# Optimization experiments

Hardware: AMD Instinct MI355X
Metric: run time of the kernel (lower is better)

The kernel has to match this reference:

```python
import jax, jax.numpy as jnp
import numpy as np

B, L, E, H = 4, 4096, 1024, 16
DH = E // H          # 64 head dim
R, M, P = 1, 8, 16   # quadrature nodes, prf features, poly sketch dim
EPS = 1e-6
C = 2.0 + EPS


def setup_inputs() -> dict:
    key = jax.random.key(0)
    ks = jax.random.split(key, 10)
    x = jax.random.normal(ks[0], (B, L, E), dtype=jnp.float32)
    qkv_w = jax.random.normal(ks[1], (E, 3 * E), dtype=jnp.float32) * 0.02
    qkv_b = jnp.zeros((3 * E,), dtype=jnp.float32)
    out_w = jax.random.normal(ks[2], (E, E), dtype=jnp.float32) * 0.02
    out_b = jnp.zeros((E,), dtype=jnp.float32)
    omega = jax.random.normal(ks[3], (R, H, DH, M), dtype=jnp.float32)
    ts_hash1 = jax.random.randint(ks[4], (DH,), 0, P)
    ts_sign1 = jax.random.randint(ks[5], (DH,), 0, 2) * 2 - 1
    ts_hash2 = jax.random.randint(ks[6], (DH,), 0, P)
    ts_sign2 = jax.random.randint(ks[7], (DH,), 0, 2) * 2 - 1
    # laggauss(1): node=1.0, weight=1.0
    quad_nodes = jnp.array([1.0], dtype=jnp.float32) / C
    quad_weights = jnp.array([1.0], dtype=jnp.float32) / C
    return {"x": x, "qkv_w": qkv_w, "qkv_b": qkv_b, "out_w": out_w,
            "out_b": out_b, "omega": omega, "quad_nodes": quad_nodes,
            "quad_weights": quad_weights, "ts_hash1": ts_hash1,
            "ts_sign1": ts_sign1, "ts_hash2": ts_hash2, "ts_sign2": ts_sign2}


def _safe_normalize(x, eps=1e-6):
    norm = jnp.linalg.norm(x, axis=-1, keepdims=True)
    return x / jnp.clip(norm, eps)


def _count_sketch(x, h, s):
    # x: (B,H,L,DH); h,s: (DH,) int
    vals = x * s.astype(x.dtype)
    Mhot = jax.nn.one_hot(h, P, dtype=x.dtype)  # (DH, P)
    return jnp.dot(vals, Mhot)                  # (B,H,L,P)


def _poly_tensor_sketch(x, h1, s1, h2, s2):
    cs1 = _count_sketch(x, h1, s1)
    cs2 = _count_sketch(x, h2, s2)
    f1 = jnp.fft.rfft(cs1, axis=-1)
    f2 = jnp.fft.rfft(cs2, axis=-1)
    ts = jnp.fft.irfft(f1 * f2, n=P, axis=-1)
    return ts / jnp.sqrt(float(P))


def _prf_features(x, omega, quad_nodes):
    proj = jnp.einsum('bhld,rhdm->rbhlm', x, omega)
    s_vals = quad_nodes.reshape(-1, 1, 1, 1, 1)
    sqrt_2s = jnp.sqrt(2.0 * jnp.clip(s_vals, 0.0))
    exp_arg = jnp.clip(proj * sqrt_2s - s_vals, -10.0, 10.0)
    return jnp.exp(exp_arg) / jnp.sqrt(float(M))


def reference(x, qkv_w, qkv_b, out_w, out_b, omega, quad_nodes, quad_weights,
              ts_hash1, ts_sign1, ts_hash2, ts_sign2):
    qkv = x @ qkv_w + qkv_b
    q, k, v = jnp.split(qkv, 3, axis=-1)
    q = q.reshape(B, L, H, DH).transpose(0, 2, 1, 3)
    k = k.reshape(B, L, H, DH).transpose(0, 2, 1, 3)
    v = v.reshape(B, L, H, DH).transpose(0, 2, 1, 3)

    q_norm = _safe_normalize(q)
    k_norm = _safe_normalize(k)

    q_poly = _poly_tensor_sketch(q_norm, ts_hash1, ts_sign1, ts_hash2, ts_sign2)
    k_poly = _poly_tensor_sketch(k_norm, ts_hash1, ts_sign1, ts_hash2, ts_sign2)
    q_prf = _prf_features(q_norm, omega, quad_nodes)
    k_prf = _prf_features(k_norm, omega, quad_nodes)

    sq_w = jnp.sqrt(jnp.clip(quad_weights.reshape(-1, 1, 1, 1, 1), 0.0))
    q_prf = q_prf * sq_w
    k_prf = k_prf * sq_w

    q_fuse = jnp.einsum('bhlp,rbhlm->bhlrpm', q_poly, q_prf).reshape(B, H, L, -1)
    k_fuse = jnp.einsum('bhlp,rbhlm->bhlrpm', k_poly, k_prf).reshape(B, H, L, -1)

    kv = jnp.einsum('bhlf,bhld->bhfd', k_fuse, v)
    context = jnp.einsum('bhlf,bhfd->bhld', q_fuse, kv)
    k_sum = k_fuse.sum(axis=2)                              # (B,H,F)
    norm = jnp.einsum('bhlf,bhf->bhl', q_fuse, k_sum)
    output = context / jnp.clip(norm, 0.0001)[..., None]

    output = output.transpose(0, 2, 1, 3).reshape(B, L, E)
    return output @ out_w + out_b
```

## Files before the change

kernel.cpp:

```cpp
#include <hip/hip_runtime.h>

typedef unsigned short u16;
typedef __attribute__((ext_vector_type(8))) short bfrag8;
typedef __attribute__((ext_vector_type(4))) float f32x4;

__device__ __forceinline__ float b2f(u16 u){ union { unsigned ui; float f; } v; v.ui = ((unsigned)u) << 16; return v.f; }
__device__ __forceinline__ u16 f2b(float f){ union { float f; unsigned ui; } v; v.f = f; unsigned r = (v.ui + 0x7FFF + ((v.ui >> 16) & 1)) >> 16; return (u16)r; }

__global__ __launch_bounds__(256) void zero_f32(float* p, int n){
  int i = blockIdx.x*256 + threadIdx.x;
  if (i < n) p[i] = 0.f;
}

__global__ __launch_bounds__(256) void transpose_f32(const float* __restrict__ W, float* __restrict__ Wt, int K, int N){
  __shared__ float tile[32][33];
  int bx = blockIdx.x * 32, by = blockIdx.y * 32;
  int tx = threadIdx.x & 31, ty = threadIdx.x >> 5;
  #pragma unroll
  for (int i = 0; i < 32; i += 8) tile[ty+i][tx] = W[(size_t)(by+ty+i)*N + bx+tx];
  __syncthreads();
  #pragma unroll
  for (int i = 0; i < 32; i += 8) Wt[(size_t)(bx+ty+i)*K + by+tx] = tile[tx][ty+i];
}

__global__ __launch_bounds__(256) void transpose_f2b(const float* __restrict__ W, u16* __restrict__ Wt, int K, int N){
  __shared__ u16 tile[32][33];
  int bx = blockIdx.x * 32, by = blockIdx.y * 32;
  int tx = threadIdx.x & 31, ty = threadIdx.x >> 5;
  #pragma unroll
  for (int i = 0; i < 32; i += 8) tile[ty+i][tx] = f2b(W[(size_t)(by+ty+i)*N + bx+tx]);
  __syncthreads();
  #pragma unroll
  for (int i = 0; i < 32; i += 8) Wt[(size_t)(bx+ty+i)*K + by+tx] = tile[tx][ty+i];
}

template<int NS>
__device__ __forceinline__ void stage_split(u16* lds, int off, const float* __restrict__ src){
  float v[8];
  *(float4*)v       = *(const float4*)src;
  *(float4*)(v + 4) = *(const float4*)(src + 4);
  u16 p0[8], p1[8];
  #pragma unroll
  for (int i = 0; i < 8; ++i){
    u16 a = f2b(v[i]); p0[i] = a;
    if constexpr (NS > 1){ p1[i] = f2b(v[i] - b2f(a)); }
  }
  *(uint4*)(lds + off) = *(uint4*)p0;
  if constexpr (NS > 1) *(uint4*)(lds + 4096 + off) = *(uint4*)p1;
}

template<int NPROD>
__global__ __launch_bounds__(256) void gemm_split(
    const float* __restrict__ A, int lda,
    const float* __restrict__ Bt, int bn_off,
    const float* __restrict__ bias,
    float* __restrict__ Cq, float* __restrict__ Ck, u16* __restrict__ Cv, int K)
{
  constexpr int NSA = (NPROD==3) ? 2 : 1;
  __shared__ __align__(16) u16 As[NSA*4096];
  __shared__ __align__(16) u16 Bs[NSA*4096];
  int tid = threadIdx.x, lane = tid & 63, wave = tid >> 6;
  int wm = wave >> 1, wn = wave & 1;
  int bm = blockIdx.y * 128, bn = blockIdx.x * 128;
  f32x4 acc[4][4];
  #pragma unroll
  for (int i=0;i<4;i++)
    #pragma unroll
    for (int j=0;j<4;j++)
      #pragma unroll
      for (int r=0;r<4;r++) acc[i][j][r] = 0.f;
  int mr = lane & 15, kq = (lane >> 4) * 8;
  for (int k0 = 0; k0 < K; k0 += 32) {
    #pragma unroll
    for (int v = 0; v < 2; ++v) {
      int idx = tid + v*256;
      int row = idx >> 2, col = (idx & 3) * 8;
      stage_split<NSA>(As, row*32 + col, &A [(size_t)(bm+row)*lda + k0 + col]);
      stage_split<NSA>(Bs, row*32 + col, &Bt[(size_t)(bn_off+bn+row)*K + k0 + col]);
    }
    __syncthreads();
    bfrag8 af[NSA][4], bf[NSA][4];
    #pragma unroll
    for (int s=0;s<NSA;s++){
      #pragma unroll
      for (int i=0;i<4;i++) af[s][i] = *(const bfrag8*)(&As[s*4096 + (wm*64 + i*16 + mr)*32 + kq]);
      #pragma unroll
      for (int j=0;j<4;j++) bf[s][j] = *(const bfrag8*)(&Bs[s*4096 + (wn*64 + j*16 + mr)*32 + kq]);
    }
#define MM(sa,sb) \
    { _Pragma("unroll") for (int i=0;i<4;i++){ _Pragma("unroll") for (int j=0;j<4;j++){ \
        acc[i][j] = __builtin_amdgcn_mfma_f32_16x16x32_bf16(af[sa][i], bf[sb][j], acc[i][j], 0, 0, 0); } } }
    if constexpr (NPROD == 3){ MM(0,1) MM(1,0) }
    MM(0,0)
#undef MM
    __syncthreads();
  }
  #pragma unroll
  for (int i=0;i<4;i++){
    #pragma unroll
    for (int j=0;j<4;j++){
      int col = bn_off + bn + wn*64 + j*16 + (lane & 15);
      float bv = bias[col];
      #pragma unroll
      for (int r=0;r<4;r++){
        int row = bm + wm*64 + i*16 + (lane>>4)*4 + r;
        float val = acc[i][j][r] + bv;
        if (col < 1024)      Cq[(size_t)row*1024 + col]        = val;
        else if (col < 2048) Ck[(size_t)row*1024 + (col-1024)] = val;
        else                 Cv[(size_t)row*1024 + (col-2048)] = f2b(val);
      }
    }
  }
}

__global__ __launch_bounds__(256) void gemm_b16(const u16* __restrict__ A, int lda,
    const u16* __restrict__ Bt, const float* __restrict__ bias, float* __restrict__ C, int N, int K)
{
  __shared__ __align__(16) u16 As[4096];
  __shared__ __align__(16) u16 Bs[4096];
  int tid = threadIdx.x, lane = tid & 63, wave = tid >> 6;
  int wm = wave >> 1, wn = wave & 1;
  int bm = blockIdx.y * 128, bn = blockIdx.x * 128;
  f32x4 acc[4][4];
  #pragma unroll
  for (int i=0;i<4;i++)
    #pragma unroll
    for (int j=0;j<4;j++)
      #pragma unroll
      for (int r=0;r<4;r++) acc[i][j][r] = 0.f;
  int mr = lane & 15, kq = (lane >> 4) * 8;
  for (int k0 = 0; k0 < K; k0 += 32) {
    #pragma unroll
    for (int v = 0; v < 2; ++v) {
      int idx = tid + v*256;
      int row = idx >> 2, col = (idx & 3) * 8;
      *(uint4*)(&As[row*32 + col]) = *(const uint4*)(&A[(size_t)(bm+row)*lda + k0 + col]);
      *(uint4*)(&Bs[row*32 + col]) = *(const uint4*)(&Bt[(size_t)(bn+row)*K + k0 + col]);
    }
    __syncthreads();
    bfrag8 af[4], bf[4];
    #pragma unroll
    for (int i=0;i<4;i++) af[i] = *(const bfrag8*)(&As[(wm*64 + i*16 + mr)*32 + kq]);
    #pragma unroll
    for (int j=0;j<4;j++) bf[j] = *(const bfrag8*)(&Bs[(wn*64 + j*16 + mr)*32 + kq]);
    #pragma unroll
    for (int i=0;i<4;i++)
      #pragma unroll
      for (int j=0;j<4;j++)
        acc[i][j] = __builtin_amdgcn_mfma_f32_16x16x32_bf16(af[i], bf[j], acc[i][j], 0, 0, 0);
    __syncthreads();
  }
  #pragma unroll
  for (int i=0;i<4;i++){
    #pragma unroll
    for (int j=0;j<4;j++){
      int col = bn + wn*64 + j*16 + (lane & 15);
      float bv = bias[col];
      #pragma unroll
      for (int r=0;r<4;r++){
        int row = bm + wm*64 + i*16 + (lane>>4)*4 + r;
        C[(size_t)row*N + col] = acc[i][j][r] + bv;
      }
    }
  }
}

struct __align__(16) ConsT { int b1; float sg1; int b2; float sg2; };

#define FEATS_COMPUTE(TILE, TOKA)                                                \
  float sq = 0.f;                                                                \
  _Pragma("unroll")                                                              \
  for (int dd = 0; dd < 16; ++dd){ float u = TILE[(TOKA)*65 + g*16 + dd]; sq += u*u; } \
  sq += __shfl_xor(sq, 16); sq += __shfl_xor(sq, 32);                            \
  float sc = 1.f / fmaxf(sqrtf(sq), 1e-6f);                                      \
  float cs1[16], cs2[16], pm[8];                                                 \
  _Pragma("unroll") for (int p=0;p<16;p++){ cs1[p]=0.f; cs2[p]=0.f; }            \
  _Pragma("unroll") for (int m=0;m<8;m++) pm[m]=0.f;                             \
  _Pragma("unroll")                                                              \
  for (int dd = 0; dd < 16; ++dd){                                               \
    int d = g*16 + dd;                                                           \
    float un = TILE[(TOKA)*65 + d] * sc;                                         \
    ConsT cc = cons[d];                                                          \
    float v1 = un*cc.sg1, v2 = un*cc.sg2;                                        \
    _Pragma("unroll")                                                            \
    for (int p=0;p<16;p++){ cs1[p] += (cc.b1==p)?v1:0.f; cs2[p] += (cc.b2==p)?v2:0.f; } \
    _Pragma("unroll")                                                            \
    for (int m=0;m<8;m++) pm[m] += un * oms[d*8 + m];                            \
  }                                                                              \
  _Pragma("unroll")                                                              \
  for (int p=0;p<16;p++){ cs1[p] += __shfl_xor(cs1[p],16); cs1[p] += __shfl_xor(cs1[p],32); \
                          cs2[p] += __shfl_xor(cs2[p],16); cs2[p] += __shfl_xor(cs2[p],32); } \
  _Pragma("unroll")                                                              \
  for (int m=0;m<8;m++){ pm[m] += __shfl_xor(pm[m],16); pm[m] += __shfl_xor(pm[m],32); } \
  float poly4[4];                                                                \
  _Pragma("unroll")                                                              \
  for (int pi=0;pi<4;pi++){ int p = g*4 + pi; float s = 0.f;                     \
    _Pragma("unroll") for (int a=0;a<16;a++) s += cs1[a]*cs2[(p-a)&15];          \
    poly4[pi] = s * 0.25f; }                                                     \
  float prf[8];                                                                  \
  _Pragma("unroll")                                                              \
  for (int m=0;m<8;m++){ float e = fminf(fmaxf(pm[m]*sqrt2s - s_node, -10.f), 10.f); \
    prf[m] = expf(e) * pscale; }

__global__ __launch_bounds__(256) void kfeat_kv(const float* __restrict__ kf, const u16* __restrict__ vb,
    const float* __restrict__ omega, const float* __restrict__ qn, const float* __restrict__ qw,
    const int* __restrict__ h1, const int* __restrict__ s1,
    const int* __restrict__ h2, const int* __restrict__ s2,
    float* __restrict__ kvT, float* __restrict__ ksum)
{
  __shared__ float ktile[64*65];
  __shared__ __align__(16) u16 vtile[64*64];
  __shared__ __align__(16) u16 featT[128*72];
  __shared__ float oms[64*8];
  __shared__ ConsT cons[64];
  int tid = threadIdx.x, lane = tid & 63, wave = tid >> 6;
  int bh = blockIdx.y, b = bh >> 4, h = bh & 15;
  int chunk = blockIdx.x;
  if (tid < 64) {
    ConsT c; c.b1 = h1[tid]; c.sg1 = (float)s1[tid]; c.b2 = h2[tid]; c.sg2 = (float)s2[tid];
    cons[tid] = c;
  }
  for (int i = tid; i < 512; i += 256) oms[i] = omega[h*512 + i];
  float s_node = qn[0];
  float sqrt2s = sqrtf(2.f * fmaxf(s_node, 0.f));
  float pscale = 0.35355339059327373f * sqrtf(fmaxf(qw[0], 0.f));
  int tloc = lane & 15, g = lane >> 4;
  int tokA = wave*16 + tloc;
  int wm = wave >> 1, wn = wave & 1;
  int mr = lane & 15, kq8 = (lane >> 4) * 8;
  f32x4 acc[4][2];
  #pragma unroll
  for (int i=0;i<4;i++)
    #pragma unroll
    for (int jn=0;jn<2;jn++)
      #pragma unroll
      for (int r=0;r<4;r++) acc[i][jn][r] = 0.f;
  float kacc[32];
  #pragma unroll
  for (int j=0;j<32;j++) kacc[j] = 0.f;
  for (int sub = 0; sub < 8; ++sub) {
    int base = chunk*512 + sub*64;
    __syncthreads();
    for (int idx = tid; idx < 4096; idx += 256) {
      int t = idx >> 6, d = idx & 63;
      ktile[t*65 + d] = kf[(size_t)(b*4096 + base + t)*1024 + h*64 + d];
    }
    for (int slot = tid; slot < 512; slot += 256) {
      int t = slot >> 3, o = (slot & 7) * 8;
      *(uint4*)(&vtile[t*64 + o]) = *(const uint4*)(&vb[(size_t)(b*4096 + base + t)*1024 + h*64 + o]);
    }
    __syncthreads();
    {
      FEATS_COMPUTE(ktile, tokA)
      #pragma unroll
      for (int pi=0;pi<4;pi++){
        #pragma unroll
        for (int m=0;m<8;m++){
          int f = (g*4 + pi)*8 + m;
          float v = poly4[pi]*prf[m];
          featT[f*72 + tokA] = f2b(v);
          v += __shfl_xor(v,1); v += __shfl_xor(v,2); v += __shfl_xor(v,4); v += __shfl_xor(v,8);
          if (tloc == 0) kacc[pi*8 + m] += v;
        }
      }
    }
    __syncthreads();
    #pragma unroll
    for (int k0 = 0; k0 < 64; k0 += 32) {
      bfrag8 af[4];
      #pragma unroll
      for (int i=0;i<4;i++) af[i] = *(const bfrag8*)(&featT[(wm*64 + i*16 + mr)*72 + k0 + kq8]);
      #pragma unroll
      for (int jn=0;jn<2;jn++){
        int d = wn*32 + jn*16 + mr;
        short tmp[8];
        #pragma unroll
        for (int j=0;j<8;j++) tmp[j] = (short)vtile[(k0 + kq8 + j)*64 + d];
        bfrag8 bf = *(bfrag8*)tmp;
        #pragma unroll
        for (int i=0;i<4;i++)
          acc[i][jn] = __builtin_amdgcn_mfma_f32_16x16x32_bf16(af[i], bf, acc[i][jn], 0, 0, 0);
      }
    }
  }
  #pragma unroll
  for (int i=0;i<4;i++){
    #pragma unroll
    for (int jn=0;jn<2;jn++){
      int d = wn*32 + jn*16 + (lane & 15);
      #pragma unroll
      for (int r=0;r<4;r++){
        int f = wm*64 + i*16 + (lane>>4)*4 + r;
        atomicAdd(&kvT[((size_t)bh*64 + d)*128 + f], acc[i][jn][r]);
      }
    }
  }
  if (tloc == 0){
    #pragma unroll
    for (int j=0;j<32;j++) atomicAdd(&ksum[bh*128 + g*32 + j], kacc[j]);
  }
}

__global__ __launch_bounds__(256) void qfeat_ctx(const float* __restrict__ qf,
    const float* __restrict__ omega, const float* __restrict__ qn, const float* __restrict__ qw,
    const int* __restrict__ h1, const int* __restrict__ s1,
    const int* __restrict__ h2, const int* __restrict__ s2,
    const float* __restrict__ kvT, const float* __restrict__ ksum,
    u16* __restrict__ attn)
{
  __shared__ float qtile[64*65];
  __shared__ __align__(16) u16 feat[64*136];
  __shared__ __align__(16) u16 kvsb0[64*136];
  __shared__ __align__(16) u16 kvsb1[64*136];
  __shared__ float ksums[128];
  __shared__ float nrm_s[64];
  __shared__ float oms[64*8];
  __shared__ ConsT cons[64];
  int tid = threadIdx.x, lane = tid & 63, wave = tid >> 6;
  int bh = blockIdx.y, b = bh >> 4, h = bh & 15;
  int chunk = blockIdx.x;
  if (tid < 64) {
    ConsT c; c.b1 = h1[tid]; c.sg1 = (float)s1[tid]; c.b2 = h2[tid]; c.sg2 = (float)s2[tid];
    cons[tid] = c;
  }
  for (int i = tid; i < 512; i += 256) oms[i] = omega[h*512 + i];
  for (int idx = tid; idx < 8192; idx += 256) {
    int d = idx >> 7, f = idx & 127;
    float v = kvT[((size_t)bh*64 + d)*128 + f];
    u16 b0 = f2b(v);
    kvsb0[d*136 + f] = b0;
    kvsb1[d*136 + f] = f2b(v - b2f(b0));
  }
  if (tid < 128) ksums[tid] = ksum[bh*128 + tid];
  float s_node = qn[0];
  float sqrt2s = sqrtf(2.f * fmaxf(s_node, 0.f));
  float pscale = 0.35355339059327373f * sqrtf(fmaxf(qw[0], 0.f));
  int tloc = lane & 15, g = lane >> 4;
  int tokA = wave*16 + tloc;
  int mr = lane & 15, kq8 = (lane >> 4) * 8;
  for (int sub = 0; sub < 8; ++sub) {
    int base = chunk*512 + sub*64;
    for (int idx = tid; idx < 4096; idx += 256) {
      int t = idx >> 6, d = idx & 63;
      qtile[t*65 + d] = qf[(size_t)(b*4096 + base + t)*1024 + h*64 + d];
    }
    __syncthreads();
    {
      FEATS_COMPUTE(qtile, tokA)
      float nv = 0.f;
      #pragma unroll
      for (int pi=0;pi<4;pi++){
        #pragma unroll
        for (int m=0;m<8;m++){
          int f = (g*4 + pi)*8 + m;
          float v = poly4[pi]*prf[m];
          feat[tokA*136 + f] = f2b(v);
          nv += v * ksums[f];
        }
      }
      nv += __shfl_xor(nv, 16); nv += __shfl_xor(nv, 32);
      if (lane < 16) nrm_s[tokA] = nv;
    }
    __syncthreads();
    f32x4 cacc[4];
    #pragma unroll
    for (int jn=0;jn<4;jn++)
      #pragma unroll
      for (int r=0;r<4;r++) cacc[jn][r] = 0.f;
    #pragma unroll
    for (int k0 = 0; k0 < 128; k0 += 32) {
      bfrag8 af = *(const bfrag8*)(&feat[(wave*16 + mr)*136 + k0 + kq8]);
      #pragma unroll
      for (int jn=0;jn<4;jn++){
        int d = jn*16 + mr;
        bfrag8 b0 = *(const bfrag8*)(&kvsb0[d*136 + k0 + kq8]);
        cacc[jn] = __builtin_amdgcn_mfma_f32_16x16x32_bf16(af, b0, cacc[jn], 0, 0, 0);
        bfrag8 b1 = *(const bfrag8*)(&kvsb1[d*136 + k0 + kq8]);
        cacc[jn] = __builtin_amdgcn_mfma_f32_16x16x32_bf16(af, b1, cacc[jn], 0, 0, 0);
      }
    }
    #pragma unroll
    for (int jn=0;jn<4;jn++){
      int d = jn*16 + (lane & 15);
      #pragma unroll
      for (int r=0;r<4;r++){
        int row = (lane>>4)*4 + r;
        float nrm = nrm_s[wave*16 + row];
        int tok = base + wave*16 + row;
        attn[(size_t)(b*4096 + tok)*2048 + h*64 + d] = f2b(cacc[jn][r] / fmaxf(nrm, 1e-4f));
      }
    }
  }
}

extern "C" void kernel_launch(void* const* d_in, const int* in_sizes, int n_in,
                              void* d_out, int out_size, void* d_ws, size_t ws_size,
                              hipStream_t stream)
{
  const float* x     = (const float*)d_in[0];
  const float* qkv_w = (const float*)d_in[1];
  const float* qkv_b = (const float*)d_in[2];
  const float* out_w = (const float*)d_in[3];
  const float* out_b = (const float*)d_in[4];
  const float* omega = (const float*)d_in[5];
  const float* qn    = (const float*)d_in[6];
  const float* qw    = (const float*)d_in[7];
  const int* h1 = (const int*)d_in[8];
  const int* s1 = (const int*)d_in[9];
  const int* h2 = (const int*)d_in[10];
  const int* s2 = (const int*)d_in[11];

  const size_t SZ_Q   = (size_t)16384*1024*4;
  const size_t SZ_K   = (size_t)16384*1024*4;
  const size_t SZ_V   = (size_t)16384*1024*2;
  const size_t SZ_WT1 = (size_t)3072*1024*4;
  const size_t SZ_WT2 = (size_t)1024*1024*2;
  const size_t SZ_KV  = (size_t)64*64*128*4;
  char* ws = (char*)d_ws;
  float* qf  = (float*)ws;
  float* kf  = (float*)(ws + SZ_Q);
  u16*   vb  = (u16*)  (ws + SZ_Q + SZ_K);
  float* wT1 = (float*)(ws + SZ_Q + SZ_K + SZ_V);
  u16*   wT2 = (u16*)  (ws + SZ_Q + SZ_K + SZ_V + SZ_WT1);
  float* kvT = (float*)(ws + SZ_Q + SZ_K + SZ_V + SZ_WT1 + SZ_WT2);
  float* ksp = (float*)(ws + SZ_Q + SZ_K + SZ_V + SZ_WT1 + SZ_WT2 + SZ_KV);

  int nz = (int)((SZ_KV + (size_t)64*128*4) / 4);
  zero_f32<<<(nz+255)/256, 256, 0, stream>>>(kvT, nz);
  transpose_f32<<<dim3(3072/32, 1024/32), 256, 0, stream>>>(qkv_w, wT1, 1024, 3072);
  transpose_f2b<<<dim3(1024/32, 1024/32), 256, 0, stream>>>(out_w, wT2, 1024, 1024);
  gemm_split<3><<<dim3(16, 128), 256, 0, stream>>>(x, 1024, wT1, 0, qkv_b, qf, kf, vb, 1024);
  gemm_split<1><<<dim3(8, 128), 256, 0, stream>>>(x, 1024, wT1, 2048, qkv_b, qf, kf, vb, 1024);
  kfeat_kv<<<dim3(8, 64), 256, 0, stream>>>(kf, vb, omega, qn, qw, h1, s1, h2, s2, kvT, ksp);
  qfeat_ctx<<<dim3(8, 64), 256, 0, stream>>>(qf, omega, qn, qw, h1, s1, h2, s2, kvT, ksp, (u16*)kf);
  gemm_b16<<<dim3(8, 128), 256, 0, stream>>>((const u16*)kf, 2048, wT2, out_b, (float*)d_out, 1024, 1024);
}
```

Before: 1.062 ms.

## Pre-split x and weights into bf16 hi/lo planes, stage via global_load_lds

Adds prepass kernels that convert x and the transposed qkv weight into separate bf16 high and low planes once, rather than having every GEMM tile re-convert fp32 to split bf16 in registers. The GEMMs then stage tiles straight from global memory into LDS with global_load_lds 16-byte transfers, using a k-group-major LDS layout. The aim is less redundant conversion ALU work and fewer register round-trips during staging. The cost is extra prepass kernels and extra workspace traffic for the split planes.

```diff
diff --git a/kernel.cpp b/kernel.cpp
--- a/kernel.cpp
+++ b/kernel.cpp
@@ -7,12 +7,32 @@
 __device__ __forceinline__ float b2f(u16 u){ union { unsigned ui; float f; } v; v.ui = ((unsigned)u) << 16; return v.f; }
 __device__ __forceinline__ u16 f2b(float f){ union { float f; unsigned ui; } v; v.f = f; unsigned r = (v.ui + 0x7FFF + ((v.ui >> 16) & 1)) >> 16; return (u16)r; }
 
+__device__ __forceinline__ void gl_lds16(const u16* g, u16* l){
+  __builtin_amdgcn_global_load_lds(
+      (const __attribute__((address_space(1))) unsigned*)g,
+      (__attribute__((address_space(3))) unsigned*)l, 16, 0, 0);
+}
+
 __global__ __launch_bounds__(256) void zero_f32(float* p, int n){
   int i = blockIdx.x*256 + threadIdx.x;
   if (i < n) p[i] = 0.f;
 }
 
-__global__ __launch_bounds__(256) void transpose_f32(const float* __restrict__ W, float* __restrict__ Wt, int K, int N){
+__global__ __launch_bounds__(256) void split_x(const float* __restrict__ x,
+    u16* __restrict__ xh, u16* __restrict__ xl){
+  size_t i = ((size_t)blockIdx.x*256 + threadIdx.x) * 8;
+  float v[8];
+  *(float4*)v       = *(const float4*)(x + i);
+  *(float4*)(v + 4) = *(const float4*)(x + i + 4);
+  u16 h[8], l[8];
+  #pragma unroll
+  for (int j = 0; j < 8; ++j){ u16 a = f2b(v[j]); h[j] = a; l[j] = f2b(v[j] - b2f(a)); }
+  *(uint4*)(xh + i) = *(uint4*)h;
+  *(uint4*)(xl + i) = *(uint4*)l;
+}
+
+__global__ __launch_bounds__(256) void transpose_split(const float* __restrict__ W,
+    u16* __restrict__ Th, u16* __restrict__ Tl, int K, int N){
   __shared__ float tile[32][33];
   int bx = blockIdx.x * 32, by = blockIdx.y * 32;
   int tx = threadIdx.x & 31, ty = threadIdx.x >> 5;
@@ -20,7 +40,12 @@
   for (int i = 0; i < 32; i += 8) tile[ty+i][tx] = W[(size_t)(by+ty+i)*N + bx+tx];
   __syncthreads();
   #pragma unroll
-  for (int i = 0; i < 32; i += 8) Wt[(size_t)(bx+ty+i)*K + by+tx] = tile[tx][ty+i];
+  for (int i = 0; i < 32; i += 8){
+    float v = tile[tx][ty+i];
+    u16 h = f2b(v);
+    Th[(size_t)(bx+ty+i)*K + by+tx] = h;
+    Tl[(size_t)(bx+ty+i)*K + by+tx] = f2b(v - b2f(h));
+  }
 }
 
 __global__ __launch_bounds__(256) void transpose_f2b(const float* __restrict__ W, u16* __restrict__ Wt, int K, int N){
@@ -34,31 +59,16 @@
   for (int i = 0; i < 32; i += 8) Wt[(size_t)(bx+ty+i)*K + by+tx] = tile[tx][ty+i];
 }
 
-template<int NS>
-__device__ __forceinline__ void stage_split(u16* lds, int off, const float* __restrict__ src){
-  float v[8];
-  *(float4*)v       = *(const float4*)src;
-  *(float4*)(v + 4) = *(const float4*)(src + 4);
-  u16 p0[8], p1[8];
-  #pragma unroll
-  for (int i = 0; i < 8; ++i){
-    u16 a = f2b(v[i]); p0[i] = a;
-    if constexpr (NS > 1){ p1[i] = f2b(v[i] - b2f(a)); }
-  }
-  *(uint4*)(lds + off) = *(uint4*)p0;
-  if constexpr (NS > 1) *(uint4*)(lds + 4096 + off) = *(uint4*)p1;
-}
-
 template<int NPROD>
-__global__ __launch_bounds__(256) void gemm_split(
-    const float* __restrict__ A, int lda,
-    const float* __restrict__ Bt, int bn_off,
+__global__ __launch_bounds__(256) void gemm_planes(
+    const u16* __restrict__ Ah, const u16* __restrict__ Al, int lda,
+    const u16* __restrict__ Bh, const u16* __restrict__ Bl, int bn_off,
     const float* __restrict__ bias,
     float* __restrict__ Cq, float* __restrict__ Ck, u16* __restrict__ Cv, int K)
 {
-  constexpr int NSA = (NPROD==3) ? 2 : 1;
-  __shared__ __align__(16) u16 As[NSA*4096];
-  __shared__ __align__(16) u16 Bs[NSA*4096];
+  constexpr int NS = (NPROD==3) ? 2 : 1;
+  __shared__ __align__(16) u16 As[NS*4096];
+  __shared__ __align__(16) u16 Bs[NS*4096];
   int tid = threadIdx.x, lane = tid & 63, wave = tid >> 6;
   int wm = wave >> 1, wn = wave & 1;
   int bm = blockIdx.y * 128, bn = blockIdx.x * 128;
@@ -69,23 +79,36 @@
     for (int j=0;j<4;j++)
       #pragma unroll
       for (int r=0;r<4;r++) acc[i][j][r] = 0.f;
-  int mr = lane & 15, kq = (lane >> 4) * 8;
+  int mr = lane & 15, g = lane >> 4;
+  int srow = (wave & 1)*64 + lane;
+  int kc1 = (wave >> 1)*8;
+  int kc2 = kc1 + 16;
+  const u16* gA0 = Ah + (size_t)(bm + srow)*lda;
+  const u16* gA1 = Al + (size_t)(bm + srow)*lda;
+  const u16* gB0 = Bh + (size_t)(bn_off + bn + srow)*K;
+  const u16* gB1 = Bl + (size_t)(bn_off + bn + srow)*K;
+  u16* dA1 = &As[wave*512];  u16* dA2 = &As[(wave+4)*512];
+  u16* dB1 = &Bs[wave*512];  u16* dB2 = &Bs[(wave+4)*512];
+
   for (int k0 = 0; k0 < K; k0 += 32) {
-    #pragma unroll
-    for (int v = 0; v < 2; ++v) {
-      int idx = tid + v*256;
-      int row = idx >> 2, col = (idx & 3) * 8;
-      stage_split<NSA>(As, row*32 + col, &A [(size_t)(bm+row)*lda + k0 + col]);
-      stage_split<NSA>(Bs, row*32 + col, &Bt[(size_t)(bn_off+bn+row)*K + k0 + col]);
-    }
-    __syncthreads();
-    bfrag8 af[NSA][4], bf[NSA][4];
-    #pragma unroll
-    for (int s=0;s<NSA;s++){
-      #pragma unroll
-      for (int i=0;i<4;i++) af[s][i] = *(const bfrag8*)(&As[s*4096 + (wm*64 + i*16 + mr)*32 + kq]);
-      #pragma unroll
-      for (int j=0;j<4;j++) bf[s][j] = *(const bfrag8*)(&Bs[s*4096 + (wn*64 + j*16 + mr)*32 + kq]);
+    gl_lds16(gA0 + k0 + kc1, dA1);
+    gl_lds16(gA0 + k0 + kc2, dA2);
+    gl_lds16(gB0 + k0 + kc1, dB1);
+    gl_lds16(gB0 + k0 + kc2, dB2);
+    if constexpr (NS > 1){
+      gl_lds16(gA1 + k0 + kc1, dA1 + 4096);
+      gl_lds16(gA1 + k0 + kc2, dA2 + 4096);
+      gl_lds16(gB1 + k0 + kc1, dB1 + 4096);
+      gl_lds16(gB1 + k0 + kc2, dB2 + 4096);
+    }
+    __syncthreads();
+    bfrag8 af[NS][4], bf[NS][4];
+    #pragma unroll
+    for (int s=0;s<NS;s++){
+      #pragma unroll
+      for (int i=0;i<4;i++) af[s][i] = *(const bfrag8*)(&As[s*4096 + g*1024 + (wm*64 + i*16 + mr)*8]);
+      #pragma unroll
+      for (int j=0;j<4;j++) bf[s][j] = *(const bfrag8*)(&Bs[s*4096 + g*1024 + (wn*64 + j*16 + mr)*8]);
     }
 #define MM(sa,sb) \
     { _Pragma("unroll") for (int i=0;i<4;i++){ _Pragma("unroll") for (int j=0;j<4;j++){ \
@@ -128,21 +151,24 @@
     for (int j=0;j<4;j++)
       #pragma unroll
       for (int r=0;r<4;r++) acc[i][j][r] = 0.f;
-  int mr = lane & 15, kq = (lane >> 4) * 8;
+  int mr = lane & 15, g = lane >> 4;
+  int srow = (wave & 1)*64 + lane;
+  int kc1 = (wave >> 1)*8, kc2 = kc1 + 16;
+  const u16* gA = A  + (size_t)(bm + srow)*lda;
+  const u16* gB = Bt + (size_t)(bn + srow)*K;
+  u16* dA1 = &As[wave*512];  u16* dA2 = &As[(wave+4)*512];
+  u16* dB1 = &Bs[wave*512];  u16* dB2 = &Bs[(wave+4)*512];
   for (int k0 = 0; k0 < K; k0 += 32) {
-    #pragma unroll
-    for (int v = 0; v < 2; ++v) {
-      int idx = tid + v*256;
-      int row = idx >> 2, col = (idx & 3) * 8;
-      *(uint4*)(&As[row*32 + col]) = *(const uint4*)(&A[(size_t)(bm+row)*lda + k0 + col]);
-      *(uint4*)(&Bs[row*32 + col]) = *(const uint4*)(&Bt[(size_t)(bn+row)*K + k0 + col]);
-    }
+    gl_lds16(gA + k0 + kc1, dA1);
+    gl_lds16(gA + k0 + kc2, dA2);
+    gl_lds16(gB + k0 + kc1, dB1);
+    gl_lds16(gB + k0 + kc2, dB2);
     __syncthreads();
     bfrag8 af[4], bf[4];
     #pragma unroll
-    for (int i=0;i<4;i++) af[i] = *(const bfrag8*)(&As[(wm*64 + i*16 + mr)*32 + kq]);
-    #pragma unroll
-    for (int j=0;j<4;j++) bf[j] = *(const bfrag8*)(&Bs[(wn*64 + j*16 + mr)*32 + kq]);
+    for (int i=0;i<4;i++) af[i] = *(const bfrag8*)(&As[g*1024 + (wm*64 + i*16 + mr)*8]);
+    #pragma unroll
+    for (int j=0;j<4;j++) bf[j] = *(const bfrag8*)(&Bs[g*1024 + (wn*64 + j*16 + mr)*8]);
     #pragma unroll
     for (int i=0;i<4;i++)
       #pragma unroll
@@ -410,27 +436,34 @@
   const int* h2 = (const int*)d_in[10];
   const int* s2 = (const int*)d_in[11];
 
-  const size_t SZ_Q   = (size_t)16384*1024*4;
-  const size_t SZ_K   = (size_t)16384*1024*4;
-  const size_t SZ_V   = (size_t)16384*1024*2;
-  const size_t SZ_WT1 = (size_t)3072*1024*4;
-  const size_t SZ_WT2 = (size_t)1024*1024*2;
-  const size_t SZ_KV  = (size_t)64*64*128*4;
+  const size_t SZ_Q  = (size_t)16384*1024*4;
+  const size_t SZ_K  = (size_t)16384*1024*4;
+  const size_t SZ_V  = (size_t)16384*1024*2;
+  const size_t SZ_XH = (size_t)16384*1024*2;
+  const size_t SZ_XL = (size_t)16384*1024*2;
+  const size_t SZ_WH = (size_t)3072*1024*2;
+  const size_t SZ_WL = (size_t)3072*1024*2;
+  const size_t SZ_W2 = (size_t)1024*1024*2;
+  const size_t SZ_KV = (size_t)64*64*128*4;
   char* ws = (char*)d_ws;
   float* qf  = (float*)ws;
   float* kf  = (float*)(ws + SZ_Q);
   u16*   vb  = (u16*)  (ws + SZ_Q + SZ_K);
-  float* wT1 = (float*)(ws + SZ_Q + SZ_K + SZ_V);
-  u16*   wT2 = (u16*)  (ws + SZ_Q + SZ_K + SZ_V + SZ_WT1);
-  float* kvT = (float*)(ws + SZ_Q + SZ_K + SZ_V + SZ_WT1 + SZ_WT2);
-  float* ksp = (float*)(ws + SZ_Q + SZ_K + SZ_V + SZ_WT1 + SZ_WT2 + SZ_KV);
+  u16*   xh  = (u16*)  (ws + SZ_Q + SZ_K + SZ_V);
+  u16*   xl  = (u16*)  (ws + SZ_Q + SZ_K + SZ_V + SZ_XH);
+  u16*   wTh = (u16*)  (ws + SZ_Q + SZ_K + SZ_V + SZ_XH + SZ_XL);
+  u16*   wTl = (u16*)  (ws + SZ_Q + SZ_K + SZ_V + SZ_XH + SZ_XL + SZ_WH);
+  u16*   wT2 = (u16*)  (ws + SZ_Q + SZ_K + SZ_V + SZ_XH + SZ_XL + SZ_WH + SZ_WL);
+  float* kvT = (float*)(ws + SZ_Q + SZ_K + SZ_V + SZ_XH + SZ_XL + SZ_WH + SZ_WL + SZ_W2);
+  float* ksp = (float*)(ws + SZ_Q + SZ_K + SZ_V + SZ_XH + SZ_XL + SZ_WH + SZ_WL + SZ_W2 + SZ_KV);
 
   int nz = (int)((SZ_KV + (size_t)64*128*4) / 4);
   zero_f32<<<(nz+255)/256, 256, 0, stream>>>(kvT, nz);
-  transpose_f32<<<dim3(3072/32, 1024/32), 256, 0, stream>>>(qkv_w, wT1, 1024, 3072);
+  split_x<<<(16384*1024/8)/256, 256, 0, stream>>>(x, xh, xl);
+  transpose_split<<<dim3(3072/32, 1024/32), 256, 0, stream>>>(qkv_w, wTh, wTl, 1024, 3072);
   transpose_f2b<<<dim3(1024/32, 1024/32), 256, 0, stream>>>(out_w, wT2, 1024, 1024);
-  gemm_split<3><<<dim3(16, 128), 256, 0, stream>>>(x, 1024, wT1, 0, qkv_b, qf, kf, vb, 1024);
-  gemm_split<1><<<dim3(8, 128), 256, 0, stream>>>(x, 1024, wT1, 2048, qkv_b, qf, kf, vb, 1024);
+  gemm_planes<3><<<dim3(16, 128), 256, 0, stream>>>(xh, xl, 1024, wTh, wTl, 0, qkv_b, qf, kf, vb, 1024);
+  gemm_planes<1><<<dim3(8, 128), 256, 0, stream>>>(xh, xl, 1024, wTh, wTl, 2048, qkv_b, qf, kf, vb, 1024);
   kfeat_kv<<<dim3(8, 64), 256, 0, stream>>>(kf, vb, omega, qn, qw, h1, s1, h2, s2, kvT, ksp);
   qfeat_ctx<<<dim3(8, 64), 256, 0, stream>>>(qf, omega, qn, qw, h1, s1, h2, s2, kvT, ksp, (u16*)kf);
   gemm_b16<<<dim3(8, 128), 256, 0, stream>>>((const u16*)kf, 2048, wT2, out_b, (float*)d_out, 1024, 1024);
```

Measured after the change: 991.0 us. -6.7%, faster.
